# Optimization experiments

Measured on AMD Instinct MI355X. Metric: run time of the kernel, lower is better.

## Reference

```python
import jax, jax.numpy as jnp
import numpy as np

B, S, HID = 2, 2048, 2048
H, KV, D = 16, 8, 128          # query heads, kv heads, head_dim
EPS = 1e-6
THETA = 1000000.0


def setup_inputs() -> dict:
    key = jax.random.key(0)
    ks = jax.random.split(key, 8)
    sc = 0.02
    hidden_states = jax.random.normal(ks[0], (B, S, HID), dtype=jnp.float32)
    Wq = jax.random.normal(ks[1], (HID, H * D), dtype=jnp.float32) * sc
    Wk = jax.random.normal(ks[2], (HID, KV * D), dtype=jnp.float32) * sc
    Wv = jax.random.normal(ks[3], (HID, KV * D), dtype=jnp.float32) * sc
    Wo = jax.random.normal(ks[4], (H * D, HID), dtype=jnp.float32) * sc
    q_norm_w = jnp.ones((D,), dtype=jnp.float32)
    k_norm_w = jnp.ones((D,), dtype=jnp.float32)
    positions = jnp.arange(S, dtype=jnp.int32)
    # causal mask: True = masked (j > i)
    attention_mask = jnp.triu(jnp.ones((S, S), dtype=bool), k=1)
    return {
        "hidden_states": hidden_states, "Wq": Wq, "Wk": Wk, "Wv": Wv,
        "Wo": Wo, "q_norm_w": q_norm_w, "k_norm_w": k_norm_w,
        "positions": positions, "attention_mask": attention_mask,
    }


def _rms_norm(x, w):
    # x: [..., D]; RMSNorm over last dim
    var = jnp.mean(x * x, axis=-1, keepdims=True)
    return x * jax.lax.rsqrt(var + EPS) * w


def _rope(x, positions):
    # x: [B, h, S, D]; standard rotate-half RoPE
    inv_freq = 1.0 / (THETA ** (jnp.arange(0, D, 2, dtype=jnp.float32) / D))
    ang = positions.astype(jnp.float32)[:, None] * inv_freq[None, :]  # [S, D/2]
    cos = jnp.concatenate([jnp.cos(ang), jnp.cos(ang)], axis=-1)      # [S, D]
    sin = jnp.concatenate([jnp.sin(ang), jnp.sin(ang)], axis=-1)
    x1, x2 = x[..., : D // 2], x[..., D // 2:]
    rot = jnp.concatenate([-x2, x1], axis=-1)
    return x * cos + rot * sin


def reference(hidden_states, Wq, Wk, Wv, Wo, q_norm_w, k_norm_w,
              positions, attention_mask):
    b, s, _ = hidden_states.shape
    q = (hidden_states @ Wq).reshape(b, s, H, D).transpose(0, 2, 1, 3)   # [B,H,S,D]
    k = (hidden_states @ Wk).reshape(b, s, KV, D).transpose(0, 2, 1, 3)  # [B,KV,S,D]
    v = (hidden_states @ Wv).reshape(b, s, KV, D).transpose(0, 2, 1, 3)
    q = _rms_norm(q, q_norm_w)
    k = _rms_norm(k, k_norm_w)
    q = _rope(q, positions)
    k = _rope(k, positions)
    # GQA: repeat kv heads
    g = H // KV
    k = jnp.repeat(k, g, axis=1)  # [B,H,S,D]
    v = jnp.repeat(v, g, axis=1)
    scale = 1.0 / np.sqrt(D).astype(np.float32)
    scores = jnp.einsum('bhqd,bhkd->bhqk', q, k) * scale
    scores = jnp.where(attention_mask[None, None, :, :], -jnp.inf, scores)
    attn = jax.nn.softmax(scores, axis=-1)
    out = jnp.einsum('bhqk,bhkd->bhqd', attn, v)
    out = out.transpose(0, 2, 1, 3).reshape(b, s, H * D)
    return out @ Wo
```

## Files before the change

### kernel.cpp

```cpp
#include <hip/hip_runtime.h>
#include <hip/hip_bf16.h>

typedef __hip_bfloat16 bf16;
typedef __attribute__((ext_vector_type(8))) short short8v;
typedef __attribute__((ext_vector_type(4))) float f32x4;

constexpr int nB = 2;
constexpr int nS = 2048;
constexpr int nHID = 2048;
constexpr int nH = 16;
constexpr int nKV = 8;
constexpr int nD = 128;
constexpr int QS = 4096;
constexpr float kEps = 1e-6f;
constexpr float kScale = 0.08838834764831845f;

template <int N>
struct IC {
  static constexpr int value = N;
};

__device__ inline float b2f(unsigned short u) {
  return __uint_as_float(((unsigned)u) << 16);
}
__device__ inline float bf2f(bf16 v) { return __bfloat162float(v); }
__device__ inline short f2bs(float f) {
  bf16 h = __float2bfloat16(f);
  return *reinterpret_cast<short*>(&h);
}
__device__ inline unsigned pack2bf(float a, float b) {
  return ((unsigned)(unsigned short)f2bs(b) << 16) |
         (unsigned)(unsigned short)f2bs(a);
}

__device__ inline void gload_lds16(const bf16* g, bf16* l) {
  __builtin_amdgcn_global_load_lds(
      (const __attribute__((address_space(1))) void*)g,
      (__attribute__((address_space(3))) void*)l, 16, 0, 0);
}

template <int N>
__device__ inline void vwait() {
  asm volatile("s_waitcnt vmcnt(%0)" ::"n"(N) : "memory");
}

__global__ __launch_bounds__(256) void cvt_f32_bf16(
    const float* __restrict__ src, bf16* __restrict__ dst, int n) {
  const int i = (blockIdx.x * 256 + threadIdx.x) * 4;
  if (i >= n) return;
  const float4 v = *reinterpret_cast<const float4*>(src + i);
  ushort4 o;
  o.x = (unsigned short)f2bs(v.x);
  o.y = (unsigned short)f2bs(v.y);
  o.z = (unsigned short)f2bs(v.z);
  o.w = (unsigned short)f2bs(v.w);
  *reinterpret_cast<ushort4*>(dst + i) = o;
}

__global__ __launch_bounds__(64) void rope_table(float2* __restrict__ tab) {
  const int s = blockIdx.x, j = threadIdx.x;
  const float invf = expf(-(float)j * (13.815510557964274f / 64.0f));
  const float ang = (float)s * invf;
  tab[s * 64 + j] = make_float2(cosf(ang), sinf(ang));
}

__global__ __launch_bounds__(256) void transpose_all(
    const float* __restrict__ Wq, const float* __restrict__ Wk,
    const float* __restrict__ Wv, const float* __restrict__ Wo,
    bf16* __restrict__ Wcat, bf16* __restrict__ Wot) {
  int t = blockIdx.x;
  const float* src;
  bf16* dst;
  int N;
  if (t < 4096) {
    src = Wq; dst = Wcat; N = 2048;
  } else if (t < 6144) {
    t -= 4096; src = Wk; dst = Wcat + (size_t)2048 * 2048; N = 1024;
  } else if (t < 8192) {
    t -= 6144; src = Wv; dst = Wcat + (size_t)3072 * 2048; N = 1024;
  } else {
    t -= 8192; src = Wo; dst = Wot; N = 2048;
  }
  const int tilesN = N >> 5;
  const int n0 = (t % tilesN) * 32, k0 = (t / tilesN) * 32;
  __shared__ float tb[32][33];
  const int c = threadIdx.x & 31, r8 = threadIdx.x >> 5;
#pragma unroll
  for (int i = 0; i < 4; ++i)
    tb[r8 + i * 8][c] = src[(size_t)(k0 + r8 + i * 8) * N + n0 + c];
  __syncthreads();
#pragma unroll
  for (int i = 0; i < 4; ++i)
    dst[(size_t)(n0 + r8 + i * 8) * 2048 + k0 + c] =
        __float2bfloat16(tb[c][r8 + i * 8]);
}

template <int BM, typename OUT_T>
__global__ __launch_bounds__(512) void gemm_8ph(
    const bf16* __restrict__ A, const bf16* __restrict__ Bt,
    OUT_T* __restrict__ C, int M, int N, int K) {
  constexpr int LA = BM / 128;
  constexpr int LB = 2;
  constexpr int MF = BM / 32;
  constexpr int MFH = MF / 2;
  constexpr int W = 2 * (LA + LB);
  constexpr int LDSB = 2 * BM * 32 + 2 * 256 * 32;
  __shared__ bf16 lds[2 * LDSB];

  const int tid = threadIdx.x;
  const int wave = tid >> 6, lane = tid & 63;
  const int lr = lane & 15, lg = lane >> 4;
  const int wm = wave >> 2, wn = wave & 3;
  const int m0 = blockIdx.y * BM, n0 = blockIdx.x * 256;
  const int srow = tid >> 2;
  const int scol = (((tid & 3) ^ ((tid >> 3) & 3)) << 3);
  const int fsw = (lr >> 1) & 3;

  auto stageA = [&](int t, int kk) {
    bf16* dst = lds + (t & 1) * LDSB + kk * (BM * 32) + wave * 512;
    const bf16* src = A + (size_t)(m0 + srow) * K + t * 64 + kk * 32 + scol;
#pragma unroll
    for (int j = 0; j < LA; ++j)
      gload_lds16(src + (size_t)(j * 128) * K, dst + j * 4096);
  };
  auto stageB = [&](int t, int kk) {
    bf16* dst =
        lds + (t & 1) * LDSB + 2 * BM * 32 + kk * (256 * 32) + wave * 512;
    const bf16* src = Bt + (size_t)(n0 + srow) * K + t * 64 + kk * 32 + scol;
#pragma unroll
    for (int j = 0; j < LB; ++j)
      gload_lds16(src + (size_t)(j * 128) * K, dst + j * 4096);
  };

  f32x4 acc[MF][4];
#pragma unroll
  for (int m = 0; m < MF; ++m)
#pragma unroll
    for (int n = 0; n < 4; ++n) acc[m][n] = (f32x4){0.f, 0.f, 0.f, 0.f};
  short8v bfr[4];

  auto phase = [&](auto WC, int buf, int kk, int mh, auto stageFn) {
    constexpr int WAIT = decltype(WC)::value;
    if constexpr (WAIT >= 0) vwait<WAIT>();
    __builtin_amdgcn_s_barrier();
    asm volatile("" ::: "memory");
    if (mh == 0) {
      const bf16* bb = lds + buf * LDSB + 2 * BM * 32 + kk * (256 * 32);
#pragma unroll
      for (int ni = 0; ni < 4; ++ni)
        bfr[ni] = *reinterpret_cast<const short8v*>(
            bb + (wn * 64 + ni * 16 + lr) * 32 + ((lg ^ fsw) << 3));
    }
    short8v af[MFH];
    const bf16* ab = lds + buf * LDSB + kk * (BM * 32);
#pragma unroll
    for (int ii = 0; ii < MFH; ++ii)
      af[ii] = *reinterpret_cast<const short8v*>(
          ab + (wm * (BM / 2) + (mh * MFH + ii) * 16 + lr) * 32 +
          ((lg ^ fsw) << 3));
    stageFn();
    asm volatile("s_waitcnt lgkmcnt(0)" ::: "memory");
    __builtin_amdgcn_sched_barrier(0);
    __builtin_amdgcn_s_setprio(1);
#pragma unroll
    for (int ii = 0; ii < MFH; ++ii)
#pragma unroll
      for (int ni = 0; ni < 4; ++ni)
        acc[mh * MFH + ii][ni] = __builtin_amdgcn_mfma_f32_16x16x32_bf16(
            af[ii], bfr[ni], acc[mh * MFH + ii][ni], 0, 0, 0);
    __builtin_amdgcn_s_setprio(0);
  };

  const int NT = K / 64;
  stageA(0, 0);
  stageB(0, 0);
  stageA(0, 1);
  stageB(0, 1);
  stageA(1, 0);
  stageB(1, 0);

  for (int t = 0; t < NT - 1; ++t) {
    const int buf = t & 1;
    phase(IC<W>{}, buf, 0, 0, [&] { stageA(t + 1, 1); });
    phase(IC<-1>{}, buf, 0, 1, [&] { stageB(t + 1, 1); });
    phase(IC<W>{}, buf, 1, 0, [&] {
      if (t < NT - 2) stageA(t + 2, 0);
    });
    phase(IC<-1>{}, buf, 1, 1, [&] {
      if (t < NT - 2) stageB(t + 2, 0);
    });
  }
  {
    const int buf = (NT - 1) & 1;
    phase(IC<LA + LB>{}, buf, 0, 0, [&] {});
    phase(IC<-1>{}, buf, 0, 1, [&] {});
    phase(IC<0>{}, buf, 1, 0, [&] {});
    phase(IC<-1>{}, buf, 1, 1, [&] {});
  }

#pragma unroll
  for (int m = 0; m < MF; ++m)
#pragma unroll
    for (int n = 0; n < 4; ++n)
#pragma unroll
      for (int r = 0; r < 4; ++r) {
        const int row = m0 + wm * (BM / 2) + m * 16 + 4 * lg + r;
        const int col = n0 + wn * 64 + n * 16 + lr;
        if constexpr (sizeof(OUT_T) == 2)
          C[(size_t)row * N + col] = __float2bfloat16(acc[m][n][r]);
        else
          C[(size_t)row * N + col] = acc[m][n][r];
      }
}

__global__ __launch_bounds__(128) void norm_rope_fused(
    bf16* __restrict__ qkv, const float* __restrict__ qw,
    const float* __restrict__ kw, const float2* __restrict__ tab) {
  const int row = blockIdx.x;
  const int head = blockIdx.y;
  const int t = threadIdx.x;
  const int s = row & (nS - 1);
  const bool isQ = head < nH;
  const int col = isQ ? head * nD : 2048 + (head - nH) * nD;
  const float* w = isQ ? qw : kw;
  bf16* xp = qkv + (size_t)row * QS + col;
  const float v = bf2f(xp[t]);
  float ss = v * v;
#pragma unroll
  for (int off = 32; off > 0; off >>= 1) ss += __shfl_xor(ss, off);
  __shared__ float wsum[2];
  __shared__ float buf[nD];
  if ((t & 63) == 0) wsum[t >> 6] = ss;
  __syncthreads();
  const float inv = rsqrtf((wsum[0] + wsum[1]) * (1.0f / nD) + kEps);
  const float nv = v * inv * w[t];
  buf[t] = nv;
  __syncthreads();
  const float partner = buf[t ^ 64];
  const float rot = (t < 64) ? -partner : partner;
  const int j = t & 63;
  const float2 cs = tab[s * 64 + j];
  const float outv = nv * cs.x + rot * cs.y;
  xp[t] = __float2bfloat16(outv);
}

constexpr int BQ = 128, BKT = 64;

__global__ __launch_bounds__(512) void attn_mfma(
    const bf16* __restrict__ QKV, bf16* __restrict__ O) {
  const int l = blockIdx.x;
  const int bh = l & 31;
  const int rr0 = l >> 5;
  const int qb = (rr0 < 8) ? 15 - rr0 : rr0 - 8;
  const int b = bh >> 4, h = bh & 15, kvh = h >> 1;
  const int q0 = qb * BQ;
  const int nt = 2 * qb + 2;
  const int tid = threadIdx.x;
  const int wave = tid >> 6, lane = tid & 63;
  const int lr = lane & 15, lg = lane >> 4;

  __shared__ bf16 Ks[BKT][136];
  __shared__ bf16 Vt[nD][72];
  __shared__ bf16 Pl[8][16][72];

  const bf16* Qbase = QKV + (size_t)b * nS * QS + h * nD;
  const bf16* Kbase = QKV + (size_t)b * nS * QS + 2048 + kvh * nD;
  const bf16* Vbase = QKV + (size_t)b * nS * QS + 3072 + kvh * nD;

  const int krow = tid >> 3, kcc = (tid & 7) * 16;
  const int vkey = tid & 63, vdc = (tid >> 6) * 16;

  short8v kreg[2], vreg[2];
  auto gload = [&](int kt) {
    const bf16* ksrc = Kbase + (size_t)(kt + krow) * QS + kcc;
    const bf16* vsrc = Vbase + (size_t)(kt + vkey) * QS + vdc;
    kreg[0] = *reinterpret_cast<const short8v*>(ksrc);
    kreg[1] = *reinterpret_cast<const short8v*>(ksrc + 8);
    vreg[0] = *reinterpret_cast<const short8v*>(vsrc);
    vreg[1] = *reinterpret_cast<const short8v*>(vsrc + 8);
  };
  auto lwrite = [&]() {
    *reinterpret_cast<short8v*>(&Ks[krow][kcc]) = kreg[0];
    *reinterpret_cast<short8v*>(&Ks[krow][kcc + 8]) = kreg[1];
#pragma unroll
    for (int i = 0; i < 2; ++i)
#pragma unroll
      for (int j = 0; j < 8; ++j)
        *reinterpret_cast<short*>(&Vt[vdc + 8 * i + j][vkey]) = vreg[i][j];
  };

  short8v qf[4];
  {
    const bf16* qrow = Qbase + (size_t)(q0 + 16 * wave + lr) * QS;
#pragma unroll
    for (int dc = 0; dc < 4; ++dc)
      qf[dc] = *reinterpret_cast<const short8v*>(qrow + 32 * dc + 8 * lg);
  }

  f32x4 of[8];
#pragma unroll
  for (int n = 0; n < 8; ++n) of[n] = (f32x4){0.f, 0.f, 0.f, 0.f};
  float m_run = -1e30f, l_run = 0.f;

  gload(0);
  lwrite();
  __syncthreads();

  for (int j = 0; j < nt; ++j) {
    const int kt = j * BKT;
    const bool have_next = (j + 1 < nt);
    if (have_next) gload((j + 1) * BKT);

    f32x4 s[4];
    __builtin_amdgcn_s_setprio(1);
#pragma unroll
    for (int sub = 0; sub < 4; ++sub) {
      f32x4 acc = {0.f, 0.f, 0.f, 0.f};
#pragma unroll
      for (int dc = 0; dc < 4; ++dc) {
        const short8v kf = *reinterpret_cast<const short8v*>(
            &Ks[16 * sub + lr][32 * dc + 8 * lg]);
        acc = __builtin_amdgcn_mfma_f32_16x16x32_bf16(kf, qf[dc], acc, 0, 0, 0);
      }
      s[sub] = acc;
    }
    __builtin_amdgcn_s_setprio(0);

    const bool needMask = (kt + BKT > q0 + 16 * wave);
#pragma unroll
    for (int sub = 0; sub < 4; ++sub)
#pragma unroll
      for (int r = 0; r < 4; ++r) {
        float v = s[sub][r] * kScale;
        if (needMask && (kt + 16 * sub + 4 * lg + r > q0 + 16 * wave + lr))
          v = -1e30f;
        s[sub][r] = v;
      }

    float pmax = -1e30f;
#pragma unroll
    for (int sub = 0; sub < 4; ++sub)
#pragma unroll
      for (int r = 0; r < 4; ++r) pmax = fmaxf(pmax, s[sub][r]);
    pmax = fmaxf(pmax, __shfl_xor(pmax, 16));
    pmax = fmaxf(pmax, __shfl_xor(pmax, 32));

    if (!__all(pmax - m_run <= 8.f)) {
      const float mt = fmaxf(m_run, pmax);
      const float corr = __expf(m_run - mt);
#pragma unroll
      for (int n = 0; n < 8; ++n) of[n] *= corr;
      l_run *= corr;
      m_run = mt;
    }

    float p[4][4];
    float lsum = 0.f;
#pragma unroll
    for (int sub = 0; sub < 4; ++sub)
#pragma unroll
      for (int r = 0; r < 4; ++r) {
        const float e = __expf(s[sub][r] - m_run);
        p[sub][r] = e;
        lsum += e;
      }
    lsum += __shfl_xor(lsum, 16);
    lsum += __shfl_xor(lsum, 32);
    l_run += lsum;

#pragma unroll
    for (int sub = 0; sub < 4; ++sub)
#pragma unroll
      for (int rp = 0; rp < 2; ++rp)
        *reinterpret_cast<unsigned*>(
            &Pl[wave][lr][16 * sub + 4 * lg + 2 * rp]) =
            pack2bf(p[sub][2 * rp], p[sub][2 * rp + 1]);

    __builtin_amdgcn_s_setprio(1);
#pragma unroll
    for (int kk = 0; kk < 2; ++kk) {
      const short8v pb =
          *reinterpret_cast<const short8v*>(&Pl[wave][lr][32 * kk + 8 * lg]);
#pragma unroll
      for (int n = 0; n < 8; ++n) {
        const short8v vf = *reinterpret_cast<const short8v*>(
            &Vt[16 * n + lr][32 * kk + 8 * lg]);
        of[n] = __builtin_amdgcn_mfma_f32_16x16x32_bf16(vf, pb, of[n], 0, 0, 0);
      }
    }
    __builtin_amdgcn_s_setprio(0);

    if (have_next) {
      __syncthreads();
      lwrite();
      __syncthreads();
    }
  }

  {
    const float inv = 1.0f / l_run;
    bf16* orow = O + ((size_t)(b * nS + q0 + 16 * wave + lr)) * (nH * nD) +
                 h * nD + 4 * lg;
#pragma unroll
    for (int n = 0; n < 8; ++n)
#pragma unroll
      for (int rp = 0; rp < 2; ++rp)
        *reinterpret_cast<unsigned*>(orow + 16 * n + 2 * rp) =
            pack2bf(of[n][2 * rp] * inv, of[n][2 * rp + 1] * inv);
  }
}

extern "C" void kernel_launch(void* const* d_in, const int* in_sizes, int n_in,
                              void* d_out, int out_size, void* d_ws,
                              size_t ws_size, hipStream_t stream) {
  const float* hs = (const float*)d_in[0];
  const float* Wq = (const float*)d_in[1];
  const float* Wk = (const float*)d_in[2];
  const float* Wv = (const float*)d_in[3];
  const float* Wo = (const float*)d_in[4];
  const float* qw = (const float*)d_in[5];
  const float* kw = (const float*)d_in[6];

  const int M = nB * nS;
  char* ws = (char*)d_ws;
  size_t off = 0;
  auto alloc = [&](size_t bytes) {
    char* p = ws + off;
    off += bytes;
    return p;
  };
  bf16* hsb = (bf16*)alloc((size_t)M * nHID * 2);
  bf16* att = hsb;
  bf16* qkv = (bf16*)alloc((size_t)M * QS * 2);
  bf16* Wcat = (bf16*)alloc((size_t)QS * nHID * 2);
  bf16* Wot = (bf16*)alloc((size_t)nH * nD * nHID * 2);
  float2* tab = (float2*)alloc((size_t)nS * 64 * 8);
  float* out = (float*)d_out;

  const int nHsElems = M * nHID;
  rope_table<<<dim3(nS), 64, 0, stream>>>(tab);
  cvt_f32_bf16<<<(nHsElems / 4 + 255) / 256, 256, 0, stream>>>(hs, hsb,
                                                               nHsElems);
  transpose_all<<<dim3(12288), 256, 0, stream>>>(Wq, Wk, Wv, Wo, Wcat, Wot);

  gemm_8ph<256, bf16><<<dim3(QS / 256, M / 256), 512, 0, stream>>>(
      hsb, Wcat, qkv, M, QS, nHID);

  norm_rope_fused<<<dim3(M, nH + nKV), 128, 0, stream>>>(qkv, qw, kw, tab);

  attn_mfma<<<dim3(512), 512, 0, stream>>>(qkv, att);

  gemm_8ph<128, float><<<dim3(nHID / 256, M / 128), 512, 0, stream>>>(
      att, Wot, out, M, nHID, nH * nD);
}
```

Measured before the change: 255.4 us.

## Add dedicated QKV GEMM with 64-wide K tiles and interleaved staging

Replaces the generic 8-phase GEMM for the QKV projection with a specialized kernel. It uses 64-wide K tiles in a double-buffered LDS layout with an XOR swizzle, and splits each tile's compute into quarter phases that each issue one async global-to-LDS stage load. The goal is to halve the number of K iterations and barriers and to overlap loads with MFMA work more evenly. It uses more LDS per block (128KB), which may limit occupancy to one block per CU.

```diff
diff --git a/kernel.cpp b/kernel.cpp
--- a/kernel.cpp
+++ b/kernel.cpp
@@ -95,6 +95,117 @@
         __float2bfloat16(tb[c][r8 + i * 8]);
 }
 
+__global__ __launch_bounds__(512) void gemm_qkv(
+    const bf16* __restrict__ A, const bf16* __restrict__ Bt,
+    bf16* __restrict__ C, int M, int N, int K) {
+  __shared__ bf16 lds[2][2][2][128 * 64];
+  const int tid = threadIdx.x;
+  const int wave = tid >> 6, lane = tid & 63;
+  const int lr = lane & 15, lg = lane >> 4;
+  const int wm = wave >> 2, wn = wave & 3;
+  const int m0 = blockIdx.y * 256, n0 = blockIdx.x * 256;
+
+  const int srow = tid >> 3;
+  const int csrc = (tid & 7) ^ ((srow & 4) >> 1);
+  const bf16* aBase = A + (size_t)m0 * K;
+  const bf16* bBase = Bt + (size_t)n0 * K;
+
+  auto stage = [&](int op, int t, int h) {
+    const bf16* base = op ? bBase : aBase;
+    bf16* dst = &lds[t & 1][op][h][(size_t)srow * 64 + (tid & 7) * 8];
+    const bf16* src = base + (size_t)(h * 128 + srow) * K + t * 64 + csrc * 8;
+    gload_lds16(src, dst);
+    gload_lds16(src + (size_t)64 * K, dst + 64 * 64);
+  };
+
+  auto readA = [&](int buf, int mi, int kk) {
+    const int rh = mi * 16 + lr;
+    return *reinterpret_cast<const short8v*>(
+        &lds[buf][0][wm][rh * 64 + ((kk * 32 + lg * 8) ^ ((rh & 4) << 2))]);
+  };
+  auto readB = [&](int buf, int ni, int kk) {
+    const int rh = (wn & 1) * 64 + ni * 16 + lr;
+    return *reinterpret_cast<const short8v*>(
+        &lds[buf][1][wn >> 1][rh * 64 + ((kk * 32 + lg * 8) ^ ((rh & 4) << 2))]);
+  };
+
+  f32x4 acc[8][4];
+#pragma unroll
+  for (int m = 0; m < 8; ++m)
+#pragma unroll
+    for (int n = 0; n < 4; ++n) acc[m][n] = (f32x4){0.f, 0.f, 0.f, 0.f};
+  short8v aF[4][2], bF[2][2];
+
+  auto phase = [&](int buf, int mh, int nh, auto stageFn, int vw) {
+    if (nh == 0) {
+#pragma unroll
+      for (int i = 0; i < 4; ++i)
+#pragma unroll
+        for (int kk = 0; kk < 2; ++kk) aF[i][kk] = readA(buf, mh * 4 + i, kk);
+    }
+#pragma unroll
+    for (int j = 0; j < 2; ++j)
+#pragma unroll
+      for (int kk = 0; kk < 2; ++kk) bF[j][kk] = readB(buf, nh * 2 + j, kk);
+    stageFn();
+    if (vw == 2)
+      vwait<2>();
+    else if (vw == 0)
+      vwait<0>();
+    __builtin_amdgcn_sched_barrier(0);
+    __builtin_amdgcn_s_barrier();
+    asm volatile("s_waitcnt lgkmcnt(0)" ::: "memory");
+    __builtin_amdgcn_sched_barrier(0);
+    __builtin_amdgcn_s_setprio(1);
+#pragma unroll
+    for (int i = 0; i < 4; ++i)
+#pragma unroll
+      for (int j = 0; j < 2; ++j)
+#pragma unroll
+        for (int kk = 0; kk < 2; ++kk)
+          acc[mh * 4 + i][nh * 2 + j] = __builtin_amdgcn_mfma_f32_16x16x32_bf16(
+              aF[i][kk], bF[j][kk], acc[mh * 4 + i][nh * 2 + j], 0, 0, 0);
+    __builtin_amdgcn_s_setprio(0);
+    __builtin_amdgcn_s_barrier();
+  };
+
+  const int NT = K / 64;
+  stage(0, 0, 0);
+  stage(0, 0, 1);
+  stage(1, 0, 0);
+  stage(1, 0, 1);
+  stage(0, 1, 0);
+  stage(0, 1, 1);
+  stage(1, 1, 0);
+  stage(1, 1, 1);
+  vwait<8>();
+  __builtin_amdgcn_s_barrier();
+
+  for (int i = 0; i < NT / 2; ++i) {
+    const int tb = 2 * i + 1, t2 = 2 * i + 2, t3 = 2 * i + 3;
+    const bool s2 = t2 < NT, s3 = t3 < NT;
+    phase(0, 0, 0, [&] { if (i > 0) stage(0, tb, 1); }, -1);
+    phase(0, 0, 1, [&] { if (i > 0) stage(1, tb, 0); }, -1);
+    phase(0, 1, 0, [&] { if (i > 0) stage(1, tb, 1); }, -1);
+    phase(0, 1, 1, [&] { if (s2) stage(0, t2, 0); }, s2 ? 2 : 0);
+    phase(1, 0, 0, [&] { if (s2) stage(0, t2, 1); }, -1);
+    phase(1, 0, 1, [&] { if (s2) stage(1, t2, 0); }, -1);
+    phase(1, 1, 0, [&] { if (s2) stage(1, t2, 1); }, -1);
+    phase(1, 1, 1, [&] { if (s3) stage(0, t3, 0); }, s3 ? 2 : 0);
+  }
+
+#pragma unroll
+  for (int m = 0; m < 8; ++m)
+#pragma unroll
+    for (int n = 0; n < 4; ++n)
+#pragma unroll
+      for (int r = 0; r < 4; ++r) {
+        const int row = m0 + wm * 128 + m * 16 + 4 * lg + r;
+        const int col = n0 + wn * 64 + n * 16 + lr;
+        C[(size_t)row * N + col] = __float2bfloat16(acc[m][n][r]);
+      }
+}
+
 template <int BM, typename OUT_T>
 __global__ __launch_bounds__(512) void gemm_8ph(
     const bf16* __restrict__ A, const bf16* __restrict__ Bt,
@@ -443,8 +554,8 @@
                                                                nHsElems);
   transpose_all<<<dim3(12288), 256, 0, stream>>>(Wq, Wk, Wv, Wo, Wcat, Wot);
 
-  gemm_8ph<256, bf16><<<dim3(QS / 256, M / 256), 512, 0, stream>>>(
-      hsb, Wcat, qkv, M, QS, nHID);
+  gemm_qkv<<<dim3(QS / 256, M / 256), 512, 0, stream>>>(hsb, Wcat, qkv, M, QS,
+                                                        nHID);
 
   norm_rope_fused<<<dim3(M, nH + nKV), 128, 0, stream>>>(qkv, qw, kw, tab);
 
```

Measured after the change: 262.5 us. 2.8% more time.

## Merge preprocessing kernels and fuse Q RMSNorm+RoPE into attention Q load

Applied to the files above, without the earlier changes.

Combines the weight transpose, hidden-state conversion, and RoPE table kernels into a single launch dispatched by block index. Moves query RMSNorm and RoPE into the attention kernel's Q-fragment load, leaving a separate norm/rope pass only for K heads. This removes launch overhead and a full read/write pass over the Q projection, at the cost of extra per-thread register work and table loads in the attention prologue.

```diff
diff --git a/kernel.cpp b/kernel.cpp
--- a/kernel.cpp
+++ b/kernel.cpp
@@ -44,55 +44,54 @@
   asm volatile("s_waitcnt vmcnt(%0)" ::"n"(N) : "memory");
 }
 
-__global__ __launch_bounds__(256) void cvt_f32_bf16(
-    const float* __restrict__ src, bf16* __restrict__ dst, int n) {
-  const int i = (blockIdx.x * 256 + threadIdx.x) * 4;
-  if (i >= n) return;
-  const float4 v = *reinterpret_cast<const float4*>(src + i);
-  ushort4 o;
-  o.x = (unsigned short)f2bs(v.x);
-  o.y = (unsigned short)f2bs(v.y);
-  o.z = (unsigned short)f2bs(v.z);
-  o.w = (unsigned short)f2bs(v.w);
-  *reinterpret_cast<ushort4*>(dst + i) = o;
-}
-
-__global__ __launch_bounds__(64) void rope_table(float2* __restrict__ tab) {
-  const int s = blockIdx.x, j = threadIdx.x;
-  const float invf = expf(-(float)j * (13.815510557964274f / 64.0f));
-  const float ang = (float)s * invf;
-  tab[s * 64 + j] = make_float2(cosf(ang), sinf(ang));
-}
-
-__global__ __launch_bounds__(256) void transpose_all(
-    const float* __restrict__ Wq, const float* __restrict__ Wk,
-    const float* __restrict__ Wv, const float* __restrict__ Wo,
-    bf16* __restrict__ Wcat, bf16* __restrict__ Wot) {
+__global__ __launch_bounds__(256) void preproc(
+    const float* __restrict__ hs, const float* __restrict__ Wq,
+    const float* __restrict__ Wk, const float* __restrict__ Wv,
+    const float* __restrict__ Wo, bf16* __restrict__ hsb,
+    bf16* __restrict__ Wcat, bf16* __restrict__ Wot,
+    float2* __restrict__ tab) {
   int t = blockIdx.x;
-  const float* src;
-  bf16* dst;
-  int N;
-  if (t < 4096) {
-    src = Wq; dst = Wcat; N = 2048;
-  } else if (t < 6144) {
-    t -= 4096; src = Wk; dst = Wcat + (size_t)2048 * 2048; N = 1024;
-  } else if (t < 8192) {
-    t -= 6144; src = Wv; dst = Wcat + (size_t)3072 * 2048; N = 1024;
+  if (t < 12288) {
+    const float* src;
+    bf16* dst;
+    int N;
+    if (t < 4096) {
+      src = Wq; dst = Wcat; N = 2048;
+    } else if (t < 6144) {
+      t -= 4096; src = Wk; dst = Wcat + (size_t)2048 * 2048; N = 1024;
+    } else if (t < 8192) {
+      t -= 6144; src = Wv; dst = Wcat + (size_t)3072 * 2048; N = 1024;
+    } else {
+      t -= 8192; src = Wo; dst = Wot; N = 2048;
+    }
+    const int tilesN = N >> 5;
+    const int n0 = (t % tilesN) * 32, k0 = (t / tilesN) * 32;
+    __shared__ float tb[32][33];
+    const int c = threadIdx.x & 31, r8 = threadIdx.x >> 5;
+#pragma unroll
+    for (int i = 0; i < 4; ++i)
+      tb[r8 + i * 8][c] = src[(size_t)(k0 + r8 + i * 8) * N + n0 + c];
+    __syncthreads();
+#pragma unroll
+    for (int i = 0; i < 4; ++i)
+      dst[(size_t)(n0 + r8 + i * 8) * 2048 + k0 + c] =
+          __float2bfloat16(tb[c][r8 + i * 8]);
+  } else if (t < 20480) {
+    const int i = ((t - 12288) * 256 + threadIdx.x) * 4;
+    const float4 v = *reinterpret_cast<const float4*>(hs + i);
+    ushort4 o;
+    o.x = (unsigned short)f2bs(v.x);
+    o.y = (unsigned short)f2bs(v.y);
+    o.z = (unsigned short)f2bs(v.z);
+    o.w = (unsigned short)f2bs(v.w);
+    *reinterpret_cast<ushort4*>(hsb + i) = o;
   } else {
-    t -= 8192; src = Wo; dst = Wot; N = 2048;
-  }
-  const int tilesN = N >> 5;
-  const int n0 = (t % tilesN) * 32, k0 = (t / tilesN) * 32;
-  __shared__ float tb[32][33];
-  const int c = threadIdx.x & 31, r8 = threadIdx.x >> 5;
-#pragma unroll
-  for (int i = 0; i < 4; ++i)
-    tb[r8 + i * 8][c] = src[(size_t)(k0 + r8 + i * 8) * N + n0 + c];
-  __syncthreads();
-#pragma unroll
-  for (int i = 0; i < 4; ++i)
-    dst[(size_t)(n0 + r8 + i * 8) * 2048 + k0 + c] =
-        __float2bfloat16(tb[c][r8 + i * 8]);
+    const int idx = (t - 20480) * 256 + threadIdx.x;
+    const int s = idx >> 6, j = idx & 63;
+    const float invf = expf(-(float)j * (13.815510557964274f / 64.0f));
+    const float ang = (float)s * invf;
+    tab[idx] = make_float2(cosf(ang), sinf(ang));
+  }
 }
 
 template <int BM, typename OUT_T>
@@ -213,17 +212,14 @@
       }
 }
 
-__global__ __launch_bounds__(128) void norm_rope_fused(
-    bf16* __restrict__ qkv, const float* __restrict__ qw,
-    const float* __restrict__ kw, const float2* __restrict__ tab) {
+__global__ __launch_bounds__(128) void norm_rope_k(
+    bf16* __restrict__ qkv, const float* __restrict__ kw,
+    const float2* __restrict__ tab) {
   const int row = blockIdx.x;
   const int head = blockIdx.y;
   const int t = threadIdx.x;
   const int s = row & (nS - 1);
-  const bool isQ = head < nH;
-  const int col = isQ ? head * nD : 2048 + (head - nH) * nD;
-  const float* w = isQ ? qw : kw;
-  bf16* xp = qkv + (size_t)row * QS + col;
+  bf16* xp = qkv + (size_t)row * QS + 2048 + head * nD;
   const float v = bf2f(xp[t]);
   float ss = v * v;
 #pragma unroll
@@ -233,7 +229,7 @@
   if ((t & 63) == 0) wsum[t >> 6] = ss;
   __syncthreads();
   const float inv = rsqrtf((wsum[0] + wsum[1]) * (1.0f / nD) + kEps);
-  const float nv = v * inv * w[t];
+  const float nv = v * inv * kw[t];
   buf[t] = nv;
   __syncthreads();
   const float partner = buf[t ^ 64];
@@ -247,7 +243,8 @@
 constexpr int BQ = 128, BKT = 64;
 
 __global__ __launch_bounds__(512) void attn_mfma(
-    const bf16* __restrict__ QKV, bf16* __restrict__ O) {
+    const bf16* __restrict__ QKV, bf16* __restrict__ O,
+    const float* __restrict__ qw, const float2* __restrict__ tab) {
   const int l = blockIdx.x;
   const int bh = l & 31;
   const int rr0 = l >> 5;
@@ -291,10 +288,45 @@
 
   short8v qf[4];
   {
-    const bf16* qrow = Qbase + (size_t)(q0 + 16 * wave + lr) * QS;
-#pragma unroll
-    for (int dc = 0; dc < 4; ++dc)
-      qf[dc] = *reinterpret_cast<const short8v*>(qrow + 32 * dc + 8 * lg);
+    const int qrow_i = q0 + 16 * wave + lr;
+    const bf16* qrow = Qbase + (size_t)qrow_i * QS;
+    float x[4][8];
+    float ss = 0.f;
+#pragma unroll
+    for (int dc = 0; dc < 4; ++dc) {
+      const short8v raw =
+          *reinterpret_cast<const short8v*>(qrow + 32 * dc + 8 * lg);
+#pragma unroll
+      for (int j2 = 0; j2 < 8; ++j2) {
+        const float v = b2f((unsigned short)raw[j2]);
+        x[dc][j2] = v;
+        ss += v * v;
+      }
+    }
+    ss += __shfl_xor(ss, 16);
+    ss += __shfl_xor(ss, 32);
+    const float inv = rsqrtf(ss * (1.0f / nD) + kEps);
+#pragma unroll
+    for (int dc = 0; dc < 4; ++dc) {
+      const float4 w0 = *reinterpret_cast<const float4*>(qw + 32 * dc + 8 * lg);
+      const float4 w1 =
+          *reinterpret_cast<const float4*>(qw + 32 * dc + 8 * lg + 4);
+      const float wv[8] = {w0.x, w0.y, w0.z, w0.w, w1.x, w1.y, w1.z, w1.w};
+#pragma unroll
+      for (int j2 = 0; j2 < 8; ++j2) x[dc][j2] *= inv * wv[j2];
+    }
+#pragma unroll
+    for (int dc = 0; dc < 4; ++dc) {
+      short8v q8;
+#pragma unroll
+      for (int j2 = 0; j2 < 8; ++j2) {
+        const int c = 32 * dc + 8 * lg + j2;
+        const float2 cs = tab[qrow_i * 64 + (c & 63)];
+        const float rot = (dc < 2) ? -x[dc ^ 2][j2] : x[dc ^ 2][j2];
+        q8[j2] = f2bs(x[dc][j2] * cs.x + rot * cs.y);
+      }
+      qf[dc] = q8;
+    }
   }
 
   f32x4 of[8];
@@ -437,18 +469,15 @@
   float2* tab = (float2*)alloc((size_t)nS * 64 * 8);
   float* out = (float*)d_out;
 
-  const int nHsElems = M * nHID;
-  rope_table<<<dim3(nS), 64, 0, stream>>>(tab);
-  cvt_f32_bf16<<<(nHsElems / 4 + 255) / 256, 256, 0, stream>>>(hs, hsb,
-                                                               nHsElems);
-  transpose_all<<<dim3(12288), 256, 0, stream>>>(Wq, Wk, Wv, Wo, Wcat, Wot);
+  preproc<<<dim3(20992), 256, 0, stream>>>(hs, Wq, Wk, Wv, Wo, hsb, Wcat, Wot,
+                                           tab);
 
   gemm_8ph<256, bf16><<<dim3(QS / 256, M / 256), 512, 0, stream>>>(
       hsb, Wcat, qkv, M, QS, nHID);
 
-  norm_rope_fused<<<dim3(M, nH + nKV), 128, 0, stream>>>(qkv, qw, kw, tab);
-
-  attn_mfma<<<dim3(512), 512, 0, stream>>>(qkv, att);
+  norm_rope_k<<<dim3(M, nKV), 128, 0, stream>>>(qkv, kw, tab);
+
+  attn_mfma<<<dim3(512), 512, 0, stream>>>(qkv, att, qw, tab);
 
   gemm_8ph<128, float><<<dim3(nHID / 256, M / 128), 512, 0, stream>>>(
       att, Wot, out, M, nHID, nH * nD);
```

New measurement: 217.8 us, median of 3. -14.7%, faster.
